# Optimization experiments

Measured on AMD Instinct MI355X. Metric: run time of the kernel, lower is better.

The kernel has to match this reference:

```python
import jax, jax.numpy as jnp
import numpy as np

N_NODES = 10000
N_EDGES = 160000
IN_CH = 256
HIDDEN = 512
N_LAYERS = 2
W_SCALE = 0.05  # keep relu chain numerically tame


def setup_inputs() -> dict:
    key = jax.random.key(0)
    ks = jax.random.split(key, 8)
    x = jax.random.normal(ks[0], (N_NODES, IN_CH), dtype=jnp.float32)
    edge_index = jax.random.randint(ks[1], (2, N_EDGES), 0, N_NODES, dtype=jnp.int64)
    W_in = jax.random.normal(ks[2], (IN_CH, HIDDEN), dtype=jnp.float32) * W_SCALE
    b_in = jnp.zeros((HIDDEN,), jnp.float32)
    msg_W = jax.random.normal(ks[3], (N_LAYERS, HIDDEN, HIDDEN), dtype=jnp.float32) * W_SCALE
    msg_b = jnp.zeros((N_LAYERS, HIDDEN), jnp.float32)
    upd_W = jax.random.normal(ks[4], (N_LAYERS, 2 * HIDDEN, HIDDEN), dtype=jnp.float32) * W_SCALE
    upd_b = jnp.zeros((N_LAYERS, HIDDEN), jnp.float32)
    W_out = jax.random.normal(ks[5], (HIDDEN, 1), dtype=jnp.float32) * W_SCALE
    b_out = jnp.zeros((1,), jnp.float32)
    return {"x": x, "edge_index": edge_index, "W_in": W_in, "b_in": b_in,
            "msg_W": msg_W, "msg_b": msg_b, "upd_W": upd_W, "upd_b": upd_b,
            "W_out": W_out, "b_out": b_out}


def reference(x, edge_index, W_in, b_in, msg_W, msg_b, upd_W, upd_b, W_out, b_out):
    src = edge_index[0]  # x_j source nodes (PyG source_to_target flow)
    dst = edge_index[1]  # aggregate into destination nodes
    n = x.shape[0]
    h = jax.nn.relu(x @ W_in + b_in)  # [N, H]
    for l in range(msg_W.shape[0]):
        # message: relu(Linear(x_j)) on gathered source features  [E, H]
        m = jax.nn.relu(h[src] @ msg_W[l] + msg_b[l])
        # aggr='add': scatter-add over destination nodes  [N, H]
        aggr = jax.ops.segment_sum(m, dst, num_segments=n)
        # update: relu(Linear(concat([x, aggr])))  [N, H]
        h = jax.nn.relu(jnp.concatenate([h, aggr], axis=-1) @ upd_W[l] + upd_b[l])
    out = h @ W_out + b_out  # [N, 1]
    return out.squeeze(-1)
```

## Files before the change

### kernel.cpp

```cpp
#include <hip/hip_runtime.h>


typedef _Float16 half8 __attribute__((ext_vector_type(8)));
typedef float float4v __attribute__((ext_vector_type(4)));

#define ASYNC_COPY16(gptr, lptr)                                              \
    __builtin_amdgcn_global_load_lds(                                         \
        (const __attribute__((address_space(1))) void*)(gptr),                \
        (__attribute__((address_space(3))) void*)(lptr), 16, 0, 0)


template<bool PIN, bool PACKC, bool OUT, int KTA, int KTW, int KTW0>
__device__ __forceinline__ void gemm_body(int id,
    const _Float16* __restrict__ A,
    const _Float16* __restrict__ Wt,
    const float* __restrict__ bias, _Float16* __restrict__ C,
    int M, int Mtiles,
    const _Float16* __restrict__ Pin,
    const float* __restrict__ Wout, const float* __restrict__ bout,
    float* __restrict__ outp)
{
    __shared__ _Float16 As[4096];
    __shared__ _Float16 Bs[4096];

    const int tid  = threadIdx.x;
    const int wave = tid >> 6, lane = tid & 63;

    const int cxcd = id & 7, j = id >> 3;
    const int mt = cxcd + 8 * (j >> 3);
    if (mt >= Mtiles) return;
    const int pn = j & 7;
    const int bm = mt * 64, bn = pn * 64;

    const int wr = (wave >> 1) * 32, wc = (wave & 1) * 32;
    const int m16 = lane & 15, quad = lane >> 4;

    float4v acc[2][2] = {};
    if (PIN) {
        const _Float16* Pt = Pin + (size_t)(mt * 8 + pn) * 4096
                                 + wave * 64 + lane;
        #pragma unroll
        for (int i = 0; i < 2; ++i)
            #pragma unroll
            for (int j2 = 0; j2 < 2; ++j2)
                #pragma unroll
                for (int rg = 0; rg < 4; ++rg)
                    acc[i][j2][rg] = (float)Pt[((i * 2 + j2) * 4 + rg) * 256];
    }
    float bv[2];
    #pragma unroll
    for (int jj = 0; jj < 2; ++jj) bv[jj] = bias[bn + wc + jj * 16 + m16];

    for (int kt = 0; kt < KTA; ++kt) {
        const _Float16* Ab = A  + (size_t)(mt * KTA + kt) * 4096;
        const _Float16* Wb = Wt + (size_t)(pn * KTW + KTW0 + kt) * 4096;
        #pragma unroll
        for (int t = 0; t < 2; ++t) {
            const int q = t * 4 + wave;
            ASYNC_COPY16(Ab + q * 512 + lane * 8, (char*)As + q * 1024);
            ASYNC_COPY16(Wb + q * 512 + lane * 8, (char*)Bs + q * 1024);
        }
        __syncthreads();
        #pragma unroll
        for (int c = 0; c < 2; ++c) {
            half8 af[2], bf[2];
            #pragma unroll
            for (int i2 = 0; i2 < 2; ++i2)
                af[i2] = *(const half8*)
                    &As[((c * 4 + quad) * 64 + wr + i2 * 16 + m16) * 8];
            #pragma unroll
            for (int j2 = 0; j2 < 2; ++j2)
                bf[j2] = *(const half8*)
                    &Bs[((c * 4 + quad) * 64 + wc + j2 * 16 + m16) * 8];
            #pragma unroll
            for (int i2 = 0; i2 < 2; ++i2)
                #pragma unroll
                for (int j2 = 0; j2 < 2; ++j2)
                    acc[i2][j2] = __builtin_amdgcn_mfma_f32_16x16x32_f16(
                        af[i2], bf[j2], acc[i2][j2], 0, 0, 0);
        }
        __syncthreads();
    }

    if (OUT) {
        #pragma unroll
        for (int i = 0; i < 2; ++i)
            #pragma unroll
            for (int rg = 0; rg < 4; ++rg) {
                const int r2 = wr + i * 16 + quad * 4 + rg;
                const int row = bm + r2;
                float pr = 0.f;
                #pragma unroll
                for (int j2 = 0; j2 < 2; ++j2) {
                    float v = fmaxf(acc[i][j2][rg] + bv[j2], 0.f);
                    pr += v * Wout[bn + wc + j2 * 16 + m16];
                }
                pr += __shfl_xor(pr, 1);
                pr += __shfl_xor(pr, 2);
                pr += __shfl_xor(pr, 4);
                pr += __shfl_xor(pr, 8);
                if (m16 == 0 && row < M)
                    atomicAdd(&outp[row],
                              pr + ((pn == 0 && wc == 0) ? bout[0] : 0.f));
            }
        return;
    }

    #pragma unroll
    for (int i = 0; i < 2; ++i)
        #pragma unroll
        for (int rg = 0; rg < 4; ++rg) {
            const int r2 = wr + i * 16 + quad * 4 + rg;
            const int row = bm + r2;
            if (row >= M) continue;
            #pragma unroll
            for (int j2 = 0; j2 < 2; ++j2) {
                float v = fmaxf(acc[i][j2][rg] + bv[j2], 0.f);
                const int coff = wc + j2 * 16 + m16;
                if (PACKC) {
                    C[(size_t)((mt * 8 + pn) * 8 + (coff >> 3)) * 512
                      + r2 * 8 + (coff & 7)] = (_Float16)v;
                } else {
                    C[(size_t)row * 512 + bn + coff] = (_Float16)v;
                }
            }
        }
}

__global__ __launch_bounds__(256) void gemm_upd_pack(
    const _Float16* __restrict__ A, const _Float16* __restrict__ Wt,
    const float* __restrict__ bias, _Float16* __restrict__ C,
    int M, int Mtiles, const _Float16* __restrict__ Pin)
{
    gemm_body<true, true, false, 8, 16, 8>(blockIdx.x, A, Wt, bias, C,
        M, Mtiles, Pin, nullptr, nullptr, nullptr);
}

__global__ __launch_bounds__(256) void gemm_upd_out(
    const _Float16* __restrict__ A, const _Float16* __restrict__ Wt,
    const float* __restrict__ bias,
    int M, int Mtiles, const _Float16* __restrict__ Pin,
    const float* __restrict__ Wout, const float* __restrict__ bout,
    float* __restrict__ outp)
{
    gemm_body<true, false, true, 8, 16, 8>(blockIdx.x, A, Wt, bias, nullptr,
        M, Mtiles, Pin, Wout, bout, outp);
}

__global__ __launch_bounds__(256) void gemm_dual(
    const _Float16* __restrict__ A,
    const _Float16* __restrict__ W1,
    const _Float16* __restrict__ W2,
    const float* __restrict__ b1,
    _Float16* __restrict__ C1,
    _Float16* __restrict__ P,
    int M, int Mtiles)
{
    __shared__ _Float16 As[4096];
    __shared__ _Float16 B1s[4096];
    __shared__ _Float16 B2s[4096];

    const int id = blockIdx.x;
    const int tid  = threadIdx.x;
    const int wave = tid >> 6, lane = tid & 63;

    const int cxcd = id & 7, j = id >> 3;
    const int mt = cxcd + 8 * (j >> 3);
    if (mt >= Mtiles) return;
    const int pn = j & 7;
    const int bm = mt * 64, bn = pn * 64;

    const int wr = (wave >> 1) * 32, wc = (wave & 1) * 32;
    const int m16 = lane & 15, quad = lane >> 4;

    float4v accM[2][2] = {};
    float4v accP[2][2] = {};
    float bv[2];
    #pragma unroll
    for (int jj = 0; jj < 2; ++jj) bv[jj] = b1[bn + wc + jj * 16 + m16];

    for (int kt = 0; kt < 8; ++kt) {
        const _Float16* Ab  = A  + (size_t)(mt * 8  + kt) * 4096;
        const _Float16* W1b = W1 + (size_t)(pn * 8  + kt) * 4096;
        const _Float16* W2b = W2 + (size_t)(pn * 16 + kt) * 4096;
        #pragma unroll
        for (int t = 0; t < 2; ++t) {
            const int q = t * 4 + wave;
            ASYNC_COPY16(Ab  + q * 512 + lane * 8, (char*)As  + q * 1024);
            ASYNC_COPY16(W1b + q * 512 + lane * 8, (char*)B1s + q * 1024);
            ASYNC_COPY16(W2b + q * 512 + lane * 8, (char*)B2s + q * 1024);
        }
        __syncthreads();
        #pragma unroll
        for (int c = 0; c < 2; ++c) {
            half8 af[2], b1f[2], b2f[2];
            #pragma unroll
            for (int i2 = 0; i2 < 2; ++i2)
                af[i2] = *(const half8*)
                    &As[((c * 4 + quad) * 64 + wr + i2 * 16 + m16) * 8];
            #pragma unroll
            for (int j2 = 0; j2 < 2; ++j2) {
                b1f[j2] = *(const half8*)
                    &B1s[((c * 4 + quad) * 64 + wc + j2 * 16 + m16) * 8];
                b2f[j2] = *(const half8*)
                    &B2s[((c * 4 + quad) * 64 + wc + j2 * 16 + m16) * 8];
            }
            #pragma unroll
            for (int i2 = 0; i2 < 2; ++i2)
                #pragma unroll
                for (int j2 = 0; j2 < 2; ++j2) {
                    accM[i2][j2] = __builtin_amdgcn_mfma_f32_16x16x32_f16(
                        af[i2], b1f[j2], accM[i2][j2], 0, 0, 0);
                    accP[i2][j2] = __builtin_amdgcn_mfma_f32_16x16x32_f16(
                        af[i2], b2f[j2], accP[i2][j2], 0, 0, 0);
                }
        }
        __syncthreads();
    }

    #pragma unroll
    for (int i = 0; i < 2; ++i)
        #pragma unroll
        for (int rg = 0; rg < 4; ++rg) {
            const int r2 = wr + i * 16 + quad * 4 + rg;
            const int row = bm + r2;
            if (row >= M) continue;
            #pragma unroll
            for (int j2 = 0; j2 < 2; ++j2) {
                float v = fmaxf(accM[i][j2][rg] + bv[j2], 0.f);
                C1[(size_t)row * 512 + bn + wc + j2 * 16 + m16] = (_Float16)v;
            }
        }
    _Float16* Pt = P + (size_t)(mt * 8 + pn) * 4096 + wave * 64 + lane;
    #pragma unroll
    for (int i = 0; i < 2; ++i)
        #pragma unroll
        for (int j2 = 0; j2 < 2; ++j2)
            #pragma unroll
            for (int rg = 0; rg < 4; ++rg)
                Pt[((i * 2 + j2) * 4 + rg) * 256] = (_Float16)accP[i][j2][rg];
}

__device__ __forceinline__ void transpose_unit(
    const float* __restrict__ src, _Float16* __restrict__ dst, int R, int tb)
{
    const int rtiles = R >> 5;
    const int r0 = (tb % rtiles) * 32, c0 = (tb / rtiles) * 32;
    const int KT = R >> 6;
    __shared__ float t[32][33];
    const int tid = threadIdx.x;
    const int tx = tid & 31, ty = tid >> 5;
    #pragma unroll
    for (int i = 0; i < 32; i += 8)
        t[ty + i][tx] = src[(size_t)(r0 + ty + i) * 512 + c0 + tx];
    __syncthreads();
    if (tid < 128) {
        const int n  = c0 + (tid >> 2);
        const int k0 = r0 + (tid & 3) * 8;
        half8 o;
        #pragma unroll
        for (int j2 = 0; j2 < 8; ++j2)
            o[j2] = (_Float16)t[(tid & 3) * 8 + j2][tid >> 2];
        *(half8*)&dst[(size_t)(((n >> 6) * KT + (k0 >> 6)) * 8 + ((k0 >> 3) & 7)) * 512
                      + (n & 63) * 8] = o;
    }
}

__global__ __launch_bounds__(256) void fill_ingemm(
    const int* __restrict__ eidx, int* __restrict__ cursor,
    int* __restrict__ srcs, int E,
    const _Float16* __restrict__ xb, const _Float16* __restrict__ WinT,
    const float* __restrict__ b_in, _Float16* __restrict__ B0,
    int M, int Mtiles,
    const float* __restrict__ msg_W, _Float16* __restrict__ msgT,
    const float* __restrict__ upd_W, _Float16* __restrict__ updT)
{
    const int gemmU = ((Mtiles + 7) >> 3) * 64;
    const int fillU = (E + 255) >> 8;
    const int b = blockIdx.x;
    if (b < gemmU) {
        gemm_body<false, true, false, 4, 4, 0>(b, xb, WinT, b_in, B0,
            M, Mtiles, nullptr, nullptr, nullptr, nullptr);
        return;
    }
    if (b < gemmU + fillU) {
        const int e = (b - gemmU) * 256 + threadIdx.x;
        if (e < E) {
            const int d = eidx[E + e];
            const int pos = atomicAdd(&cursor[d], 1);
            if (pos < 64) srcs[d * 64 + pos] = eidx[e];
        }
        return;
    }
    const int tB = b - gemmU - fillU;
    if (tB < 256)       transpose_unit(msg_W,              msgT,              512,  tB);
    else if (tB < 512)  transpose_unit(msg_W + 512 * 512,  msgT + 512 * 512,  512,  tB - 256);
    else if (tB < 1024) transpose_unit(upd_W,              updT,              1024, tB - 512);
    else                transpose_unit(upd_W + 1024 * 512, updT + 512 * 1024, 1024, tB - 1024);
}

__global__ __launch_bounds__(256) void prep(
    const float* __restrict__ W_in,  _Float16* __restrict__ WinT,
    const float* __restrict__ x,     _Float16* __restrict__ xb,
    int* __restrict__ cursor, float* __restrict__ outz,
    int n4, int M)
{
    const int b = blockIdx.x;
    const int tid = threadIdx.x;
    const int castU = (n4 + 255) >> 8;
    if (b < 128) {
        transpose_unit(W_in, WinT, 256, b);
    } else if (b < 128 + castU) {
        const int i = (b - 128) * 256 + tid;
        if (i < n4) {
            const float4 v = *(const float4*)(x + (size_t)i * 4);
            ushort4 s;
            union { _Float16 h; unsigned short u; } cv;
            cv.h = (_Float16)v.x; s.x = cv.u;
            cv.h = (_Float16)v.y; s.y = cv.u;
            cv.h = (_Float16)v.z; s.z = cv.u;
            cv.h = (_Float16)v.w; s.w = cv.u;
            const int f = i * 4;
            const int m = f >> 8, k = f & 255;
            *(ushort4*)((unsigned short*)xb
                + (size_t)(((m >> 6) * 4 + (k >> 6)) * 8 + ((k >> 3) & 7)) * 512
                + (m & 63) * 8 + (k & 7)) = s;
        }
    } else {
        const int zi = (b - 128 - castU) * 256 + tid;
        if (zi < M) { cursor[zi] = 0; outz[zi] = 0.f; }
    }
}

__global__ __launch_bounds__(256) void aggregate_f16(
    const _Float16* __restrict__ hmr, const int* __restrict__ cursor,
    const int* __restrict__ srcs, _Float16* __restrict__ ag, int n)
{
    const int l16  = threadIdx.x & 15;
    const int node = blockIdx.x * 16 + (threadIdx.x >> 4);
    if (node >= n) return;
    const int c8 = blockIdx.y * 128 + l16 * 8;
    const int beg = node * 64;
    const int end = beg + min(cursor[node], 64);
    float a[8] = {};
    int j = beg;
    for (; j + 3 < end; j += 4) {
        const half8 v0 = *(const half8*)(hmr + (size_t)srcs[j]     * 512 + c8);
        const half8 v1 = *(const half8*)(hmr + (size_t)srcs[j + 1] * 512 + c8);
        const half8 v2 = *(const half8*)(hmr + (size_t)srcs[j + 2] * 512 + c8);
        const half8 v3 = *(const half8*)(hmr + (size_t)srcs[j + 3] * 512 + c8);
        #pragma unroll
        for (int i = 0; i < 8; ++i)
            a[i] += ((float)v0[i] + (float)v1[i]) + ((float)v2[i] + (float)v3[i]);
    }
    for (; j < end; ++j) {
        const half8 v = *(const half8*)(hmr + (size_t)srcs[j] * 512 + c8);
        #pragma unroll
        for (int i = 0; i < 8; ++i) a[i] += (float)v[i];
    }
    half8 o;
    #pragma unroll
    for (int i = 0; i < 8; ++i) o[i] = (_Float16)a[i];
    *(half8*)(ag + (size_t)(((node >> 6) * 8 + (c8 >> 6)) * 8 + ((c8 >> 3) & 7)) * 512
              + (node & 63) * 8) = o;
}

extern "C" void kernel_launch(void* const* d_in, const int* in_sizes, int n_in,
                              void* d_out, int out_size, void* d_ws, size_t ws_size,
                              hipStream_t stream)
{
    const float* x     = (const float*)d_in[0];
    const int*   eidx  = (const int*)  d_in[1];
    const float* W_in  = (const float*)d_in[2];
    const float* b_in  = (const float*)d_in[3];
    const float* msg_W = (const float*)d_in[4];
    const float* msg_b = (const float*)d_in[5];
    const float* upd_W = (const float*)d_in[6];
    const float* upd_b = (const float*)d_in[7];
    const float* W_out = (const float*)d_in[8];
    const float* b_out = (const float*)d_in[9];

    const int IN = 256, H = 512;
    const int M = in_sizes[0] / IN;
    const int E = in_sizes[1] / 2;
    const int Mtiles = (M + 63) / 64;
    const size_t Mt64 = (size_t)Mtiles * 64;

    _Float16* xb   = (_Float16*)d_ws;
    _Float16* B0   = xb + Mt64 * IN;
    _Float16* B1   = B0 + Mt64 * H;
    _Float16* B2   = B1 + Mt64 * H;
    _Float16* WinT = B2 + Mt64 * H;
    _Float16* msgT = WinT + (size_t)H * IN;
    _Float16* updT = msgT + (size_t)2 * H * H;
    int* cursor = (int*)(updT + (size_t)2 * H * 2 * H);
    int* srcs   = cursor + M;
    _Float16* Pbuf = (_Float16*)(srcs + (size_t)M * 64);

    const dim3 blk(256);
    const int gemmBlocks = ((Mtiles + 7) / 8) * 64;
    const dim3 aggrGrid((M + 15) / 16, 4);

    const int n4 = M * IN / 4;
    const int castU = (n4 + 255) / 256;
    const int fillU = (E + 255) / 256;
    const int zeroU = (M + 255) / 256;
    const int transU = 1536;

    prep<<<dim3(128 + castU + zeroU), blk, 0, stream>>>(
        W_in, WinT, x, xb, cursor, (float*)d_out, n4, M);
    fill_ingemm<<<dim3(gemmBlocks + fillU + transU), blk, 0, stream>>>(
        eidx, cursor, srcs, E, xb, WinT, b_in, B0, M, Mtiles,
        msg_W, msgT, upd_W, updT);

    gemm_dual<<<dim3(gemmBlocks), blk, 0, stream>>>(
        B0, msgT, updT, msg_b, B1, Pbuf, M, Mtiles);
    aggregate_f16<<<aggrGrid, blk, 0, stream>>>(B1, cursor, srcs, B2, M);
    gemm_upd_pack<<<dim3(gemmBlocks), blk, 0, stream>>>(
        B2, updT, upd_b, B1, M, Mtiles, Pbuf);
    gemm_dual<<<dim3(gemmBlocks), blk, 0, stream>>>(
        B1, msgT + 512 * 512, updT + 512 * 1024, msg_b + 512,
        B0, Pbuf, M, Mtiles);
    aggregate_f16<<<aggrGrid, blk, 0, stream>>>(B0, cursor, srcs, B2, M);
    gemm_upd_out<<<dim3(gemmBlocks), blk, 0, stream>>>(
        B2, updT + 512 * 1024, upd_b + 512, M, Mtiles, Pbuf,
        W_out, b_out, (float*)d_out);
}
```

Measured before the change: 194.9 us.

## Split dual GEMM and run update partial GEMM alongside aggregation

```diff
diff --git a/kernel.cpp b/kernel.cpp
--- a/kernel.cpp
+++ b/kernel.cpp
@@ -10,7 +10,7 @@
         (__attribute__((address_space(3))) void*)(lptr), 16, 0, 0)
 
 
-template<bool PIN, bool PACKC, bool OUT, int KTA, int KTW, int KTW0>
+template<bool PIN, int MODE, int KTA, int KTW, int KTW0>
 __device__ __forceinline__ void gemm_body(int id,
     const _Float16* __restrict__ A,
     const _Float16* __restrict__ Wt,
@@ -47,9 +47,11 @@
                 for (int rg = 0; rg < 4; ++rg)
                     acc[i][j2][rg] = (float)Pt[((i * 2 + j2) * 4 + rg) * 256];
     }
-    float bv[2];
-    #pragma unroll
-    for (int jj = 0; jj < 2; ++jj) bv[jj] = bias[bn + wc + jj * 16 + m16];
+    float bv[2] = {0.f, 0.f};
+    if (MODE != 2) {
+        #pragma unroll
+        for (int jj = 0; jj < 2; ++jj) bv[jj] = bias[bn + wc + jj * 16 + m16];
+    }
 
     for (int kt = 0; kt < KTA; ++kt) {
         const _Float16* Ab = A  + (size_t)(mt * KTA + kt) * 4096;
@@ -82,7 +84,7 @@
         __syncthreads();
     }
 
-    if (OUT) {
+    if (MODE == 3) {
         #pragma unroll
         for (int i = 0; i < 2; ++i)
             #pragma unroll
@@ -106,6 +108,18 @@
         return;
     }
 
+    if (MODE == 2) {
+        _Float16* Pt = C + (size_t)(mt * 8 + pn) * 4096 + wave * 64 + lane;
+        #pragma unroll
+        for (int i = 0; i < 2; ++i)
+            #pragma unroll
+            for (int j2 = 0; j2 < 2; ++j2)
+                #pragma unroll
+                for (int rg = 0; rg < 4; ++rg)
+                    Pt[((i * 2 + j2) * 4 + rg) * 256] = (_Float16)acc[i][j2][rg];
+        return;
+    }
+
     #pragma unroll
     for (int i = 0; i < 2; ++i)
         #pragma unroll
@@ -117,7 +131,7 @@
             for (int j2 = 0; j2 < 2; ++j2) {
                 float v = fmaxf(acc[i][j2][rg] + bv[j2], 0.f);
                 const int coff = wc + j2 * 16 + m16;
-                if (PACKC) {
+                if (MODE == 0) {
                     C[(size_t)((mt * 8 + pn) * 8 + (coff >> 3)) * 512
                       + r2 * 8 + (coff & 7)] = (_Float16)v;
                 } else {
@@ -127,12 +141,21 @@
         }
 }
 
+__global__ __launch_bounds__(256) void gemm_msg(
+    const _Float16* __restrict__ A, const _Float16* __restrict__ W1,
+    const float* __restrict__ b1, _Float16* __restrict__ C1,
+    int M, int Mtiles)
+{
+    gemm_body<false, 1, 8, 8, 0>(blockIdx.x, A, W1, b1, C1,
+        M, Mtiles, nullptr, nullptr, nullptr, nullptr);
+}
+
 __global__ __launch_bounds__(256) void gemm_upd_pack(
     const _Float16* __restrict__ A, const _Float16* __restrict__ Wt,
     const float* __restrict__ bias, _Float16* __restrict__ C,
     int M, int Mtiles, const _Float16* __restrict__ Pin)
 {
-    gemm_body<true, true, false, 8, 16, 8>(blockIdx.x, A, Wt, bias, C,
+    gemm_body<true, 0, 8, 16, 8>(blockIdx.x, A, Wt, bias, C,
         M, Mtiles, Pin, nullptr, nullptr, nullptr);
 }
 
@@ -143,102 +166,57 @@
     const float* __restrict__ Wout, const float* __restrict__ bout,
     float* __restrict__ outp)
 {
-    gemm_body<true, false, true, 8, 16, 8>(blockIdx.x, A, Wt, bias, nullptr,
+    gemm_body<true, 3, 8, 16, 8>(blockIdx.x, A, Wt, bias, nullptr,
         M, Mtiles, Pin, Wout, bout, outp);
 }
 
-__global__ __launch_bounds__(256) void gemm_dual(
-    const _Float16* __restrict__ A,
-    const _Float16* __restrict__ W1,
-    const _Float16* __restrict__ W2,
-    const float* __restrict__ b1,
-    _Float16* __restrict__ C1,
-    _Float16* __restrict__ P,
-    int M, int Mtiles)
-{
-    __shared__ _Float16 As[4096];
-    __shared__ _Float16 B1s[4096];
-    __shared__ _Float16 B2s[4096];
-
-    const int id = blockIdx.x;
+__device__ __forceinline__ void aggregate_body(
+    const _Float16* __restrict__ hmr, const int* __restrict__ cursor,
+    const int* __restrict__ srcs, _Float16* __restrict__ ag, int n, int ab)
+{
     const int tid  = threadIdx.x;
-    const int wave = tid >> 6, lane = tid & 63;
-
-    const int cxcd = id & 7, j = id >> 3;
-    const int mt = cxcd + 8 * (j >> 3);
-    if (mt >= Mtiles) return;
-    const int pn = j & 7;
-    const int bm = mt * 64, bn = pn * 64;
-
-    const int wr = (wave >> 1) * 32, wc = (wave & 1) * 32;
-    const int m16 = lane & 15, quad = lane >> 4;
-
-    float4v accM[2][2] = {};
-    float4v accP[2][2] = {};
-    float bv[2];
+    const int l16  = tid & 15;
+    const int node = (ab >> 2) * 16 + (tid >> 4);
+    if (node >= n) return;
+    const int c8 = (ab & 3) * 128 + l16 * 8;
+    const int beg = node * 64;
+    const int end = beg + min(cursor[node], 64);
+    float a[8] = {};
+    int j = beg;
+    for (; j + 3 < end; j += 4) {
+        const half8 v0 = *(const half8*)(hmr + (size_t)srcs[j]     * 512 + c8);
+        const half8 v1 = *(const half8*)(hmr + (size_t)srcs[j + 1] * 512 + c8);
+        const half8 v2 = *(const half8*)(hmr + (size_t)srcs[j + 2] * 512 + c8);
+        const half8 v3 = *(const half8*)(hmr + (size_t)srcs[j + 3] * 512 + c8);
+        #pragma unroll
+        for (int i = 0; i < 8; ++i)
+            a[i] += ((float)v0[i] + (float)v1[i]) + ((float)v2[i] + (float)v3[i]);
+    }
+    for (; j < end; ++j) {
+        const half8 v = *(const half8*)(hmr + (size_t)srcs[j] * 512 + c8);
+        #pragma unroll
+        for (int i = 0; i < 8; ++i) a[i] += (float)v[i];
+    }
+    half8 o;
     #pragma unroll
-    for (int jj = 0; jj < 2; ++jj) bv[jj] = b1[bn + wc + jj * 16 + m16];
-
-    for (int kt = 0; kt < 8; ++kt) {
-        const _Float16* Ab  = A  + (size_t)(mt * 8  + kt) * 4096;
-        const _Float16* W1b = W1 + (size_t)(pn * 8  + kt) * 4096;
-        const _Float16* W2b = W2 + (size_t)(pn * 16 + kt) * 4096;
-        #pragma unroll
-        for (int t = 0; t < 2; ++t) {
-            const int q = t * 4 + wave;
-            ASYNC_COPY16(Ab  + q * 512 + lane * 8, (char*)As  + q * 1024);
-            ASYNC_COPY16(W1b + q * 512 + lane * 8, (char*)B1s + q * 1024);
-            ASYNC_COPY16(W2b + q * 512 + lane * 8, (char*)B2s + q * 1024);
-        }
-        __syncthreads();
-        #pragma unroll
-        for (int c = 0; c < 2; ++c) {
-            half8 af[2], b1f[2], b2f[2];
-            #pragma unroll
-            for (int i2 = 0; i2 < 2; ++i2)
-                af[i2] = *(const half8*)
-                    &As[((c * 4 + quad) * 64 + wr + i2 * 16 + m16) * 8];
-            #pragma unroll
-            for (int j2 = 0; j2 < 2; ++j2) {
-                b1f[j2] = *(const half8*)
-                    &B1s[((c * 4 + quad) * 64 + wc + j2 * 16 + m16) * 8];
-                b2f[j2] = *(const half8*)
-                    &B2s[((c * 4 + quad) * 64 + wc + j2 * 16 + m16) * 8];
-            }
-            #pragma unroll
-            for (int i2 = 0; i2 < 2; ++i2)
-                #pragma unroll
-                for (int j2 = 0; j2 < 2; ++j2) {
-                    accM[i2][j2] = __builtin_amdgcn_mfma_f32_16x16x32_f16(
-                        af[i2], b1f[j2], accM[i2][j2], 0, 0, 0);
-                    accP[i2][j2] = __builtin_amdgcn_mfma_f32_16x16x32_f16(
-                        af[i2], b2f[j2], accP[i2][j2], 0, 0, 0);
-                }
-        }
-        __syncthreads();
-    }
-
-    #pragma unroll
-    for (int i = 0; i < 2; ++i)
-        #pragma unroll
-        for (int rg = 0; rg < 4; ++rg) {
-            const int r2 = wr + i * 16 + quad * 4 + rg;
-            const int row = bm + r2;
-            if (row >= M) continue;
-            #pragma unroll
-            for (int j2 = 0; j2 < 2; ++j2) {
-                float v = fmaxf(accM[i][j2][rg] + bv[j2], 0.f);
-                C1[(size_t)row * 512 + bn + wc + j2 * 16 + m16] = (_Float16)v;
-            }
-        }
-    _Float16* Pt = P + (size_t)(mt * 8 + pn) * 4096 + wave * 64 + lane;
-    #pragma unroll
-    for (int i = 0; i < 2; ++i)
-        #pragma unroll
-        for (int j2 = 0; j2 < 2; ++j2)
-            #pragma unroll
-            for (int rg = 0; rg < 4; ++rg)
-                Pt[((i * 2 + j2) * 4 + rg) * 256] = (_Float16)accP[i][j2][rg];
+    for (int i = 0; i < 8; ++i) o[i] = (_Float16)a[i];
+    *(half8*)(ag + (size_t)(((node >> 6) * 8 + (c8 >> 6)) * 8 + ((c8 >> 3) & 7)) * 512
+              + (node & 63) * 8) = o;
+}
+
+__global__ __launch_bounds__(256) void aggp(
+    const _Float16* __restrict__ hmr, const int* __restrict__ cursor,
+    const int* __restrict__ srcs, _Float16* __restrict__ ag, int n,
+    const _Float16* __restrict__ A, const _Float16* __restrict__ W2,
+    _Float16* __restrict__ P, int Mtiles, int gemmBlocks)
+{
+    const int b = blockIdx.x;
+    if (b < gemmBlocks) {
+        gemm_body<false, 2, 8, 16, 0>(b, A, W2, nullptr, P,
+            n, Mtiles, nullptr, nullptr, nullptr, nullptr);
+        return;
+    }
+    aggregate_body(hmr, cursor, srcs, ag, n, b - gemmBlocks);
 }
 
 __device__ __forceinline__ void transpose_unit(
@@ -279,7 +257,7 @@
     const int fillU = (E + 255) >> 8;
     const int b = blockIdx.x;
     if (b < gemmU) {
-        gemm_body<false, true, false, 4, 4, 0>(b, xb, WinT, b_in, B0,
+        gemm_body<false, 0, 4, 4, 0>(b, xb, WinT, b_in, B0,
             M, Mtiles, nullptr, nullptr, nullptr, nullptr);
         return;
     }
@@ -332,39 +310,6 @@
     }
 }
 
-__global__ __launch_bounds__(256) void aggregate_f16(
-    const _Float16* __restrict__ hmr, const int* __restrict__ cursor,
-    const int* __restrict__ srcs, _Float16* __restrict__ ag, int n)
-{
-    const int l16  = threadIdx.x & 15;
-    const int node = blockIdx.x * 16 + (threadIdx.x >> 4);
-    if (node >= n) return;
-    const int c8 = blockIdx.y * 128 + l16 * 8;
-    const int beg = node * 64;
-    const int end = beg + min(cursor[node], 64);
-    float a[8] = {};
-    int j = beg;
-    for (; j + 3 < end; j += 4) {
-        const half8 v0 = *(const half8*)(hmr + (size_t)srcs[j]     * 512 + c8);
-        const half8 v1 = *(const half8*)(hmr + (size_t)srcs[j + 1] * 512 + c8);
-        const half8 v2 = *(const half8*)(hmr + (size_t)srcs[j + 2] * 512 + c8);
-        const half8 v3 = *(const half8*)(hmr + (size_t)srcs[j + 3] * 512 + c8);
-        #pragma unroll
-        for (int i = 0; i < 8; ++i)
-            a[i] += ((float)v0[i] + (float)v1[i]) + ((float)v2[i] + (float)v3[i]);
-    }
-    for (; j < end; ++j) {
-        const half8 v = *(const half8*)(hmr + (size_t)srcs[j] * 512 + c8);
-        #pragma unroll
-        for (int i = 0; i < 8; ++i) a[i] += (float)v[i];
-    }
-    half8 o;
-    #pragma unroll
-    for (int i = 0; i < 8; ++i) o[i] = (_Float16)a[i];
-    *(half8*)(ag + (size_t)(((node >> 6) * 8 + (c8 >> 6)) * 8 + ((c8 >> 3) & 7)) * 512
-              + (node & 63) * 8) = o;
-}
-
 extern "C" void kernel_launch(void* const* d_in, const int* in_sizes, int n_in,
                               void* d_out, int out_size, void* d_ws, size_t ws_size,
                               hipStream_t stream)
@@ -399,7 +344,7 @@
 
     const dim3 blk(256);
     const int gemmBlocks = ((Mtiles + 7) / 8) * 64;
-    const dim3 aggrGrid((M + 15) / 16, 4);
+    const int aggrU = ((M + 15) / 16) * 4;
 
     const int n4 = M * IN / 4;
     const int castU = (n4 + 255) / 256;
@@ -413,15 +358,18 @@
         eidx, cursor, srcs, E, xb, WinT, b_in, B0, M, Mtiles,
         msg_W, msgT, upd_W, updT);
 
-    gemm_dual<<<dim3(gemmBlocks), blk, 0, stream>>>(
-        B0, msgT, updT, msg_b, B1, Pbuf, M, Mtiles);
-    aggregate_f16<<<aggrGrid, blk, 0, stream>>>(B1, cursor, srcs, B2, M);
+    gemm_msg<<<dim3(gemmBlocks), blk, 0, stream>>>(
+        B0, msgT, msg_b, B1, M, Mtiles);
+    aggp<<<dim3(gemmBlocks + aggrU), blk, 0, stream>>>(
+        B1, cursor, srcs, B2, M,
+        B0, updT, Pbuf, Mtiles, gemmBlocks);
     gemm_upd_pack<<<dim3(gemmBlocks), blk, 0, stream>>>(
         B2, updT, upd_b, B1, M, Mtiles, Pbuf);
-    gemm_dual<<<dim3(gemmBlocks), blk, 0, stream>>>(
-        B1, msgT + 512 * 512, updT + 512 * 1024, msg_b + 512,
-        B0, Pbuf, M, Mtiles);
-    aggregate_f16<<<aggrGrid, blk, 0, stream>>>(B0, cursor, srcs, B2, M);
+    gemm_msg<<<dim3(gemmBlocks), blk, 0, stream>>>(
+        B1, msgT + 512 * 512, msg_b + 512, B0, M, Mtiles);
+    aggp<<<dim3(gemmBlocks + aggrU), blk, 0, stream>>>(
+        B0, cursor, srcs, B2, M,
+        B1, updT + 512 * 1024, Pbuf, Mtiles, gemmBlocks);
     gemm_upd_out<<<dim3(gemmBlocks), blk, 0, stream>>>(
         B2, updT + 512 * 1024, upd_b + 512, M, Mtiles, Pbuf,
         W_out, b_out, (float*)d_out);
```

Measured after the change: 190.8 us. -2.1%, faster.
